# Optimization experiments

Hardware: AMD Instinct MI355X
Metric: run time of the kernel (lower is better)

The kernel has to match this reference:

```python
import jax, jax.numpy as jnp
import numpy as np
from jax import lax

D_MODEL, N_STATE, L_LEN = 1024, 64, 4096
DT_INIT = 0.1


def hippo_legs_matrix(N):
    # Standard HiPPO-LegS: A[n,k] = -sqrt(2n+1)sqrt(2k+1) if n>k, -(n+1) if n==k, 0 else
    n = np.arange(N, dtype=np.float32)
    r = np.sqrt(2.0 * n + 1.0)
    A = np.where(n[:, None] > n[None, :], r[:, None] * r[None, :], 0.0)
    A = -(A + np.diag(n + 1.0))
    B = r.copy()
    return jnp.asarray(A, jnp.float32), jnp.asarray(B, jnp.float32)


def setup_inputs() -> dict:
    key = jax.random.key(0)
    kB, kC = jax.random.split(key)
    A_ct, B_ref = hippo_legs_matrix(N_STATE)
    B0 = jnp.tile(B_ref[None, :], (D_MODEL, 1))
    B = B0 + 0.01 * jax.random.normal(kB, (D_MODEL, N_STATE), jnp.float32)
    C = jax.random.normal(kC, (D_MODEL, N_STATE), jnp.float32) * 0.1
    D = jnp.zeros((D_MODEL,), jnp.float32)
    log_dt = jnp.asarray(np.log(DT_INIT), jnp.float32)
    return {"A_ct": A_ct, "B": B, "C": C, "D": D, "log_dt": log_dt}


def reference(A_ct, B, C, D, log_dt):
    dt = jnp.exp(log_dt)
    N = A_ct.shape[0]
    I = jnp.eye(N, dtype=A_ct.dtype)
    M = I - (dt / 2.0) * A_ct          # (N,N)
    P = I + (dt / 2.0) * A_ct          # (N,N)
    A_bar = jnp.linalg.solve(M, P)     # (N,N)
    # B_bar[d] = M^{-1} (dt * B[d])  -> solve on transposed batch
    B_bar = jnp.linalg.solve(M, (dt * B).T).T  # (D,N)

    def step(x, _):
        # x: (D,N) state; emit readout then advance
        y = jnp.sum(C * x, axis=-1)    # (D,)
        return x @ A_bar.T, y

    _, ys = lax.scan(step, B_bar, None, length=L_LEN)  # ys: (L,D)
    K = ys.T                                           # (D,L)
    K = K.at[:, 0].add(D)
    return K[:, None, :]                                # (D,1,L)
```

## Files before the change

kernel.cpp:

```cpp
#include <hip/hip_runtime.h>
#include <math.h>


#define BPAD 72
#define ARR (64 * BPAD)

#define WS_BBAR   16
#define WS_SPL    65552
#define WS_MV     (WS_SPL + 12*8192)
#define WS_GT     (WS_MV + 4096)
#define WS_H      (WS_GT + 64*4096)
#define WS_W      (WS_H + 64*4096)
#define WS_X      (WS_W + 1024*4096)

using bf16x8 = __attribute__((ext_vector_type(8))) short;
using f32x4v = __attribute__((ext_vector_type(4))) float;
typedef unsigned short ushort_t;

__device__ __forceinline__ ushort_t f2bf(float x) {
  unsigned u = __builtin_bit_cast(unsigned, x);
  return (ushort_t)((u + 0x7FFFu + ((u >> 16) & 1u)) >> 16);
}
__device__ __forceinline__ float bfhi(float x) {
  unsigned u = __builtin_bit_cast(unsigned, x);
  unsigned r = (u + 0x7FFFu + ((u >> 16) & 1u)) & 0xFFFF0000u;
  return __builtin_bit_cast(float, r);
}
__device__ __forceinline__ ushort_t* usp(float* ws, int foff) {
  return (ushort_t*)(ws + foff);
}
__device__ __forceinline__ const ushort_t* uspc(const float* ws, int foff) {
  return (const ushort_t*)(ws + foff);
}

__device__ __forceinline__ void mm_frag(const ushort_t* __restrict__ Ah,
                                        const ushort_t* __restrict__ Al,
                                        const ushort_t* __restrict__ Bh,
                                        const ushort_t* __restrict__ Bl,
                                        int w, int lane, f32x4v acc[4]) {
  const int lm = lane & 15, quad = lane >> 4;
  const int ar = (16 * w + lm) * BPAD, ko = quad * 8;
#pragma unroll
  for (int nt = 0; nt < 4; ++nt) { acc[nt][0] = acc[nt][1] = acc[nt][2] = acc[nt][3] = 0.f; }
#pragma unroll
  for (int kc = 0; kc < 64; kc += 32) {
    const bf16x8 ahi = *(const bf16x8*)&Ah[ar + kc + ko];
    const bf16x8 alo = *(const bf16x8*)&Al[ar + kc + ko];
#pragma unroll
    for (int nt = 0; nt < 4; ++nt) {
      const int br = (16 * nt + lm) * BPAD + kc + ko;
      const bf16x8 bhi = *(const bf16x8*)&Bh[br];
      const bf16x8 blo = *(const bf16x8*)&Bl[br];
      acc[nt] = __builtin_amdgcn_mfma_f32_16x16x32_bf16(ahi, bhi, acc[nt], 0, 0, 0);
      acc[nt] = __builtin_amdgcn_mfma_f32_16x16x32_bf16(ahi, blo, acc[nt], 0, 0, 0);
      acc[nt] = __builtin_amdgcn_mfma_f32_16x16x32_bf16(alo, bhi, acc[nt], 0, 0, 0);
    }
  }
}

__device__ __forceinline__ void dstore_lds(const f32x4v acc[4],
                                           ushort_t* __restrict__ Ah, ushort_t* __restrict__ Al,
                                           ushort_t* __restrict__ Bth, ushort_t* __restrict__ Btl,
                                           int w, int lane) {
  const int lm = lane & 15, quad = lane >> 4;
  const int m0 = 16 * w + 4 * quad;
#pragma unroll
  for (int nt = 0; nt < 4; ++nt) {
    const int n = 16 * nt + lm;
    ushort_t h[4], l[4];
#pragma unroll
    for (int reg = 0; reg < 4; ++reg) {
      const float x = acc[nt][reg];
      h[reg] = f2bf(x); l[reg] = f2bf(x - bfhi(x));
      Ah[(m0 + reg) * BPAD + n] = h[reg];
      Al[(m0 + reg) * BPAD + n] = l[reg];
    }
    uint2 hp, lp;
    hp.x = (unsigned)h[0] | ((unsigned)h[1] << 16);
    hp.y = (unsigned)h[2] | ((unsigned)h[3] << 16);
    lp.x = (unsigned)l[0] | ((unsigned)l[1] << 16);
    lp.y = (unsigned)l[2] | ((unsigned)l[3] << 16);
    *(uint2*)&Bth[n * BPAD + m0] = hp;
    *(uint2*)&Btl[n * BPAD + m0] = lp;
  }
}

__device__ __forceinline__ void cp_l2w(const ushort_t* __restrict__ l,
                                       ushort_t* __restrict__ g, int tid) {
  for (int e = tid; e < 512; e += 256) {
    const int row = e >> 3, c8 = (e & 7) * 8;
    *(uint4*)&g[row * 64 + c8] = *(const uint4*)&l[row * BPAD + c8];
  }
}
__device__ __forceinline__ void cp_w2l(const ushort_t* __restrict__ g,
                                       ushort_t* __restrict__ l, int tid) {
  for (int e = tid; e < 512; e += 256) {
    const int row = e >> 3, c8 = (e & 7) * 8;
    *(uint4*)&l[row * BPAD + c8] = *(const uint4*)&g[row * 64 + c8];
  }
}

__device__ __forceinline__ void split_stage(const float* __restrict__ g,
                                            ushort_t* __restrict__ Ah,
                                            ushort_t* __restrict__ Al, int tid) {
#pragma unroll
  for (int j = 0; j < 4; ++j) {
    const int flat = j * 1024 + tid * 4;
    const int row = flat >> 6, col = flat & 63;
    const float4 v = *(const float4*)&g[flat];
    ushort_t h0 = f2bf(v.x), h1 = f2bf(v.y), h2 = f2bf(v.z), h3 = f2bf(v.w);
    ushort_t l0 = f2bf(v.x - bfhi(v.x)), l1 = f2bf(v.y - bfhi(v.y));
    ushort_t l2 = f2bf(v.z - bfhi(v.z)), l3 = f2bf(v.w - bfhi(v.w));
    uint2 hp, lp;
    hp.x = (unsigned)h0 | ((unsigned)h1 << 16); hp.y = (unsigned)h2 | ((unsigned)h3 << 16);
    lp.x = (unsigned)l0 | ((unsigned)l1 << 16); lp.y = (unsigned)l2 | ((unsigned)l3 << 16);
    *(uint2*)&Ah[row * BPAD + col] = hp;
    *(uint2*)&Al[row * BPAD + col] = lp;
  }
}

__global__ __launch_bounds__(256) void k_setup(const float* __restrict__ A,
                                               const float* __restrict__ logdt,
                                               float* __restrict__ ws) {
  __shared__ __align__(16) char SM[74240];
  float* Msh = (float*)SM;
  float* Tm  = (float*)(SM + 16640);
  float* tmpb = (float*)(SM + 33280);
  ushort_t* ping = (ushort_t*)(SM + 37376);
  ushort_t* pong = (ushort_t*)SM;
  const int tid = threadIdx.x;
  const int w = tid >> 6, lane = tid & 63;

  const float hdt = 0.5f * expf(logdt[0]);
  for (int idx = tid; idx < 4096; idx += 256) {
    const int i = idx >> 6, j = idx & 63;
    Msh[i * 65 + j] = ((i == j) ? 1.f : 0.f) - hdt * A[idx];
    Tm[i * 65 + j] = 0.f;
  }
  __syncthreads();
  if (tid < 64) Tm[tid * 65 + tid] = 1.0f / Msh[tid * 65 + tid];
  __syncthreads();
  for (int lb = 0; lb < 6; ++lb) {
    const int b = 1 << lb;
    const int E = 32 * b;
    for (int e = tid; e < E; e += 256) {
      const int rem = e & (b * b - 1);
      const int p = e >> (2 * lb);
      const int i = rem >> lb, j = rem & (b - 1);
      const int c0 = p << (lb + 1), r0 = c0 + b;
      float s = 0.f;
      for (int k = 0; k < b; ++k)
        s += Msh[(r0 + i) * 65 + c0 + k] * Tm[(c0 + k) * 65 + c0 + j];
      tmpb[e] = s;
    }
    __syncthreads();
    for (int e = tid; e < E; e += 256) {
      const int rem = e & (b * b - 1);
      const int p = e >> (2 * lb);
      const int i = rem >> lb, j = rem & (b - 1);
      const int c0 = p << (lb + 1), r0 = c0 + b;
      float s = 0.f;
      const float* tp = &tmpb[e - rem];
      for (int k = 0; k < b; ++k)
        s += Tm[(r0 + i) * 65 + r0 + k] * tp[k * b + j];
      Tm[(r0 + i) * 65 + c0 + j] = -s;
    }
    __syncthreads();
  }

  {
    ushort_t* MvH = usp(ws, WS_MV);
    ushort_t* MvL = usp(ws, WS_MV + 2048);
    for (int idx = tid; idx < 4096; idx += 256) {
      const int i = idx >> 6, j = idx & 63;
      const float mv = Tm[i * 65 + j];
      MvH[idx] = f2bf(mv); MvL[idx] = f2bf(mv - bfhi(mv));
      const float v = 2.f * mv - ((i == j) ? 1.f : 0.f);
      const ushort_t h = f2bf(v), l = f2bf(v - bfhi(v));
      ping[0 * ARR + i * BPAD + j] = h; ping[1 * ARR + i * BPAD + j] = l;
      ping[2 * ARR + j * BPAD + i] = h; ping[3 * ARR + j * BPAD + i] = l;
    }
  }
  __syncthreads();
  cp_l2w(ping + 0 * ARR, usp(ws, WS_SPL + 0), tid);
  cp_l2w(ping + 1 * ARR, usp(ws, WS_SPL + 2048), tid);
  cp_l2w(ping + 2 * ARR, usp(ws, WS_SPL + 4096), tid);
  cp_l2w(ping + 3 * ARR, usp(ws, WS_SPL + 6144), tid);

  ushort_t* cur = ping;
  ushort_t* nxt = pong;
  for (int sj = 1; sj < 12; ++sj) {
    f32x4v acc[4];
    mm_frag(cur, cur + ARR, cur + 2 * ARR, cur + 3 * ARR, w, lane, acc);
    dstore_lds(acc, nxt, nxt + ARR, nxt + 2 * ARR, nxt + 3 * ARR, w, lane);
    __syncthreads();
    const int base = WS_SPL + sj * 8192;
    cp_l2w(nxt + 0 * ARR, usp(ws, base + 0), tid);
    cp_l2w(nxt + 1 * ARR, usp(ws, base + 2048), tid);
    cp_l2w(nxt + 2 * ARR, usp(ws, base + 4096), tid);
    cp_l2w(nxt + 3 * ARR, usp(ws, base + 6144), tid);
    ushort_t* t = cur; cur = nxt; nxt = t;
  }
}

__global__ __launch_bounds__(256) void k_powers(const float* __restrict__ Bg,
                                                const float* __restrict__ logdt,
                                                float* __restrict__ ws) {
  __shared__ __align__(16) ushort_t SMp[8 * ARR];
  ushort_t* curA = SMp;
  ushort_t* ponA = SMp + 2 * ARR;
  ushort_t* Bst  = SMp + 4 * ARR;
  ushort_t* BtO  = SMp + 6 * ARR;
  const int p = blockIdx.x, tid = threadIdx.x;
  const int w = tid >> 6, lane = tid & 63;

  if (p < 128) {
    const int chain = p >> 6, r = p & 63;
    ushort_t* dstH = usp(ws, (chain ? WS_H : WS_GT) + r * 4096);
    ushort_t* dstL = usp(ws, (chain ? WS_H : WS_GT) + r * 4096 + 2048);
    if (r == 0) {
      for (int idx = tid; idx < 4096; idx += 256) {
        const int i = idx >> 6, j = idx & 63;
        dstH[idx] = (i == j) ? (ushort_t)0x3F80 : (ushort_t)0;
        dstL[idx] = 0;
      }
      return;
    }
    const int j0 = __ffs(r) - 1;
    if (r == (1 << j0)) {
      const int sb = WS_SPL + (chain * 6 + j0) * 8192;
      const int src = chain ? sb : (sb + 4096);
      const uint4* sh = (const uint4*)uspc(ws, src);
      const uint4* sl = (const uint4*)uspc(ws, src + 2048);
      uint4* dh = (uint4*)dstH;
      uint4* dl = (uint4*)dstL;
      for (int e = tid; e < 512; e += 256) { dh[e] = sh[e]; dl[e] = sl[e]; }
      return;
    }
    {
      const int sb = WS_SPL + (chain * 6 + j0) * 8192;
      cp_w2l(uspc(ws, sb + 0), curA, tid);
      cp_w2l(uspc(ws, sb + 2048), curA + ARR, tid);
    }
    ushort_t* ca = curA;
    ushort_t* na = ponA;
    for (int j = j0 + 1; j < 6; ++j) {
      if ((r >> j) & 1) {
        __syncthreads();
        const int sb = WS_SPL + (chain * 6 + j) * 8192;
        cp_w2l(uspc(ws, sb + 4096), Bst, tid);
        cp_w2l(uspc(ws, sb + 6144), Bst + ARR, tid);
        __syncthreads();
        f32x4v acc[4];
        mm_frag(ca, ca + ARR, Bst, Bst + ARR, w, lane, acc);
        dstore_lds(acc, na, na + ARR, BtO, BtO + ARR, w, lane);
        ushort_t* t = ca; ca = na; na = t;
      }
    }
    __syncthreads();
    if (chain == 0) {
      cp_l2w(BtO, dstH, tid);
      cp_l2w(BtO + ARR, dstL, tid);
    } else {
      cp_l2w(ca, dstH, tid);
      cp_l2w(ca + ARR, dstL, tid);
    }
  } else {
    const int d0 = (p - 128) * 64;
    const float dtv = expf(logdt[0]);
    split_stage(Bg + d0 * 64, curA, curA + ARR, tid);
    cp_w2l(uspc(ws, WS_MV), Bst, tid);
    cp_w2l(uspc(ws, WS_MV + 2048), Bst + ARR, tid);
    __syncthreads();
    f32x4v acc[4];
    mm_frag(curA, curA + ARR, Bst, Bst + ARR, w, lane, acc);
    const int lm = lane & 15, quad = lane >> 4;
    float* od = ws + WS_BBAR + d0 * 64;
#pragma unroll
    for (int nt = 0; nt < 4; ++nt)
#pragma unroll
      for (int reg = 0; reg < 4; ++reg)
        od[(16 * w + 4 * quad + reg) * 64 + 16 * nt + lm] = dtv * acc[nt][reg];
  }
}

__global__ __launch_bounds__(256) void k_expand(const float* __restrict__ Cg,
                                                float* __restrict__ ws) {
  __shared__ __align__(16) ushort_t SMe[4 * ARR];
  ushort_t* Asp = SMe;
  ushort_t* Bsp = SMe + 2 * ARR;
  const int p = blockIdx.x, tid = threadIdx.x;
  const int chain = p >> 10, rr = (p >> 4) & 63, dch = p & 15;
  const int w = tid >> 6, lane = tid & 63;
  const int d0 = dch * 64;

  split_stage(chain ? (ws + WS_BBAR + d0 * 64) : (Cg + d0 * 64), Asp, Asp + ARR, tid);
  const int mb = (chain ? WS_H : WS_GT) + rr * 4096;
  cp_w2l(uspc(ws, mb + 0), Bsp, tid);
  cp_w2l(uspc(ws, mb + 2048), Bsp + ARR, tid);
  __syncthreads();

  f32x4v acc[4];
  mm_frag(Asp, Asp + ARR, Bsp, Bsp + ARR, w, lane, acc);

  const int lm = lane & 15, quad = lane >> 4;
  float* dst = ws + (chain ? WS_X : WS_W) + d0 * 4096 + rr * 64;
#pragma unroll
  for (int nt = 0; nt < 4; ++nt)
#pragma unroll
    for (int reg = 0; reg < 4; ++reg)
      dst[(16 * w + 4 * quad + reg) * 4096 + 16 * nt + lm] = acc[nt][reg];
}

__global__ __launch_bounds__(256) void k_contract(const float* __restrict__ Dg,
                                                  const float* __restrict__ ws,
                                                  float* __restrict__ out) {
  __shared__ __align__(16) ushort_t XhiL[64 * BPAD];
  __shared__ __align__(16) ushort_t XloL[64 * BPAD];
  __shared__ __align__(16) ushort_t WhiL[64 * BPAD];
  __shared__ __align__(16) ushort_t WloL[64 * BPAD];
  const int d = blockIdx.x, tid = threadIdx.x;
  const float* Wg = ws + WS_W + d * 4096;
  const float* Xg = ws + WS_X + d * 4096;

#pragma unroll
  for (int j = 0; j < 4; ++j) {
    const int flat = j * 1024 + tid * 4;
    const int row = flat >> 6, col = flat & 63;
    const float4 wv = *(const float4*)&Wg[flat];
    const float4 xv = *(const float4*)&Xg[flat];
    const int o = row * BPAD + col;
#pragma unroll
    for (int s = 0; s < 2; ++s) {
      const float4 v = s ? xv : wv;
      ushort_t h0 = f2bf(v.x), h1 = f2bf(v.y), h2 = f2bf(v.z), h3 = f2bf(v.w);
      ushort_t l0 = f2bf(v.x - bfhi(v.x)), l1 = f2bf(v.y - bfhi(v.y));
      ushort_t l2 = f2bf(v.z - bfhi(v.z)), l3 = f2bf(v.w - bfhi(v.w));
      uint2 hp, lp;
      hp.x = (unsigned)h0 | ((unsigned)h1 << 16); hp.y = (unsigned)h2 | ((unsigned)h3 << 16);
      lp.x = (unsigned)l0 | ((unsigned)l1 << 16); lp.y = (unsigned)l2 | ((unsigned)l3 << 16);
      *(uint2*)&(s ? XhiL : WhiL)[o] = hp;
      *(uint2*)&(s ? XloL : WloL)[o] = lp;
    }
  }
  __syncthreads();

  const int w = tid >> 6, lane = tid & 63;
  const int lm = lane & 15, quad = lane >> 4;
  const int qrow = 16 * w + lm;
  const int koff = quad * 8;

  f32x4v acc[4];
#pragma unroll
  for (int nt = 0; nt < 4; ++nt) { acc[nt][0] = 0.f; acc[nt][1] = 0.f; acc[nt][2] = 0.f; acc[nt][3] = 0.f; }

#pragma unroll
  for (int kc = 0; kc < 64; kc += 32) {
    const bf16x8 ahi = *(const bf16x8*)&XhiL[qrow * BPAD + kc + koff];
    const bf16x8 alo = *(const bf16x8*)&XloL[qrow * BPAD + kc + koff];
#pragma unroll
    for (int nt = 0; nt < 4; ++nt) {
      const int rrow = 16 * nt + lm;
      const bf16x8 bhi = *(const bf16x8*)&WhiL[rrow * BPAD + kc + koff];
      const bf16x8 blo = *(const bf16x8*)&WloL[rrow * BPAD + kc + koff];
      acc[nt] = __builtin_amdgcn_mfma_f32_16x16x32_bf16(ahi, bhi, acc[nt], 0, 0, 0);
      acc[nt] = __builtin_amdgcn_mfma_f32_16x16x32_bf16(ahi, blo, acc[nt], 0, 0, 0);
      acc[nt] = __builtin_amdgcn_mfma_f32_16x16x32_bf16(alo, bhi, acc[nt], 0, 0, 0);
    }
  }

  if (tid == 0) acc[0][0] += Dg[d];

  float* od = out + d * 4096;
#pragma unroll
  for (int nt = 0; nt < 4; ++nt) {
#pragma unroll
    for (int reg = 0; reg < 4; ++reg) {
      const int q = 16 * w + quad * 4 + reg;
      od[q * 64 + 16 * nt + lm] = acc[nt][reg];
    }
  }
}

extern "C" void kernel_launch(void* const* d_in, const int* in_sizes, int n_in,
                              void* d_out, int out_size, void* d_ws, size_t ws_size,
                              hipStream_t stream) {
  const float* A     = (const float*)d_in[0];
  const float* B     = (const float*)d_in[1];
  const float* C     = (const float*)d_in[2];
  const float* Dv    = (const float*)d_in[3];
  const float* logdt = (const float*)d_in[4];
  float* ws  = (float*)d_ws;
  float* out = (float*)d_out;

  hipLaunchKernelGGL(k_setup,    dim3(1),    dim3(256), 0, stream, A, logdt, ws);
  hipLaunchKernelGGL(k_powers,   dim3(144),  dim3(256), 0, stream, B, logdt, ws);
  hipLaunchKernelGGL(k_expand,   dim3(2048), dim3(256), 0, stream, C, ws);
  hipLaunchKernelGGL(k_contract, dim3(1024), dim3(256), 0, stream, Dv, ws, out);
}
```

Baseline: 127.2 us.

## Fuse four stage kernels into one cooperative persistent kernel with grid syncs

```diff
diff --git a/kernel.cpp b/kernel.cpp
--- a/kernel.cpp
+++ b/kernel.cpp
@@ -1,5 +1,8 @@
 #include <hip/hip_runtime.h>
+#include <hip/hip_cooperative_groups.h>
 #include <math.h>
+
+namespace cg = cooperative_groups;
 
 
 #define BPAD 72
@@ -74,6 +77,47 @@
       h[reg] = f2bf(x); l[reg] = f2bf(x - bfhi(x));
       Ah[(m0 + reg) * BPAD + n] = h[reg];
       Al[(m0 + reg) * BPAD + n] = l[reg];
+    }
+    uint2 hp, lp;
+    hp.x = (unsigned)h[0] | ((unsigned)h[1] << 16);
+    hp.y = (unsigned)h[2] | ((unsigned)h[3] << 16);
+    lp.x = (unsigned)l[0] | ((unsigned)l[1] << 16);
+    lp.y = (unsigned)l[2] | ((unsigned)l[3] << 16);
+    *(uint2*)&Bth[n * BPAD + m0] = hp;
+    *(uint2*)&Btl[n * BPAD + m0] = lp;
+  }
+}
+
+__device__ __forceinline__ void dstore_A(const f32x4v acc[4],
+                                         ushort_t* __restrict__ Ah, ushort_t* __restrict__ Al,
+                                         int w, int lane) {
+  const int lm = lane & 15, quad = lane >> 4;
+  const int m0 = 16 * w + 4 * quad;
+#pragma unroll
+  for (int nt = 0; nt < 4; ++nt) {
+    const int n = 16 * nt + lm;
+#pragma unroll
+    for (int reg = 0; reg < 4; ++reg) {
+      const float x = acc[nt][reg];
+      Ah[(m0 + reg) * BPAD + n] = f2bf(x);
+      Al[(m0 + reg) * BPAD + n] = f2bf(x - bfhi(x));
+    }
+  }
+}
+
+__device__ __forceinline__ void dstore_Bt(const f32x4v acc[4],
+                                          ushort_t* __restrict__ Bth, ushort_t* __restrict__ Btl,
+                                          int w, int lane) {
+  const int lm = lane & 15, quad = lane >> 4;
+  const int m0 = 16 * w + 4 * quad;
+#pragma unroll
+  for (int nt = 0; nt < 4; ++nt) {
+    const int n = 16 * nt + lm;
+    ushort_t h[4], l[4];
+#pragma unroll
+    for (int reg = 0; reg < 4; ++reg) {
+      const float x = acc[nt][reg];
+      h[reg] = f2bf(x); l[reg] = f2bf(x - bfhi(x));
     }
     uint2 hp, lp;
     hp.x = (unsigned)h[0] | ((unsigned)h[1] << 16);
@@ -119,103 +163,110 @@
   }
 }
 
-__global__ __launch_bounds__(256) void k_setup(const float* __restrict__ A,
-                                               const float* __restrict__ logdt,
-                                               float* __restrict__ ws) {
-  __shared__ __align__(16) char SM[74240];
-  float* Msh = (float*)SM;
-  float* Tm  = (float*)(SM + 16640);
-  float* tmpb = (float*)(SM + 33280);
-  ushort_t* ping = (ushort_t*)(SM + 37376);
-  ushort_t* pong = (ushort_t*)SM;
-  const int tid = threadIdx.x;
+__global__ __launch_bounds__(256, 4) void k_fused(const float* __restrict__ A,
+                                                  const float* __restrict__ Bg,
+                                                  const float* __restrict__ Cg,
+                                                  const float* __restrict__ Dg,
+                                                  const float* __restrict__ logdt,
+                                                  float* __restrict__ ws,
+                                                  float* __restrict__ out,
+                                                  int grid) {
+  __shared__ __align__(16) char SM[37376];
+  const int bid = blockIdx.x, tid = threadIdx.x;
   const int w = tid >> 6, lane = tid & 63;
-
-  const float hdt = 0.5f * expf(logdt[0]);
-  for (int idx = tid; idx < 4096; idx += 256) {
-    const int i = idx >> 6, j = idx & 63;
-    Msh[i * 65 + j] = ((i == j) ? 1.f : 0.f) - hdt * A[idx];
-    Tm[i * 65 + j] = 0.f;
-  }
-  __syncthreads();
-  if (tid < 64) Tm[tid * 65 + tid] = 1.0f / Msh[tid * 65 + tid];
-  __syncthreads();
-  for (int lb = 0; lb < 6; ++lb) {
-    const int b = 1 << lb;
-    const int E = 32 * b;
-    for (int e = tid; e < E; e += 256) {
-      const int rem = e & (b * b - 1);
-      const int p = e >> (2 * lb);
-      const int i = rem >> lb, j = rem & (b - 1);
-      const int c0 = p << (lb + 1), r0 = c0 + b;
-      float s = 0.f;
-      for (int k = 0; k < b; ++k)
-        s += Msh[(r0 + i) * 65 + c0 + k] * Tm[(c0 + k) * 65 + c0 + j];
-      tmpb[e] = s;
-    }
-    __syncthreads();
-    for (int e = tid; e < E; e += 256) {
-      const int rem = e & (b * b - 1);
-      const int p = e >> (2 * lb);
-      const int i = rem >> lb, j = rem & (b - 1);
-      const int c0 = p << (lb + 1), r0 = c0 + b;
-      float s = 0.f;
-      const float* tp = &tmpb[e - rem];
-      for (int k = 0; k < b; ++k)
-        s += Tm[(r0 + i) * 65 + r0 + k] * tp[k * b + j];
-      Tm[(r0 + i) * 65 + c0 + j] = -s;
-    }
-    __syncthreads();
-  }
-
-  {
+  cg::grid_group gg = cg::this_grid();
+
+  if (bid == 0) {
+    float* Msh = (float*)SM;
+    float* Tm  = (float*)(SM + 16640);
+    float* tmpb = (float*)(SM + 33280);
+    ushort_t* ping = (ushort_t*)SM;
+
+    const float hdt = 0.5f * expf(logdt[0]);
+    for (int idx = tid; idx < 4096; idx += 256) {
+      const int i = idx >> 6, j = idx & 63;
+      Msh[i * 65 + j] = ((i == j) ? 1.f : 0.f) - hdt * A[idx];
+      Tm[i * 65 + j] = 0.f;
+    }
+    __syncthreads();
+    if (tid < 64) Tm[tid * 65 + tid] = 1.0f / Msh[tid * 65 + tid];
+    __syncthreads();
+    for (int lb = 0; lb < 6; ++lb) {
+      const int b = 1 << lb;
+      const int E = 32 * b;
+      for (int e = tid; e < E; e += 256) {
+        const int rem = e & (b * b - 1);
+        const int p = e >> (2 * lb);
+        const int i = rem >> lb, j = rem & (b - 1);
+        const int c0 = p << (lb + 1), r0 = c0 + b;
+        float s = 0.f;
+        for (int k = 0; k < b; ++k)
+          s += Msh[(r0 + i) * 65 + c0 + k] * Tm[(c0 + k) * 65 + c0 + j];
+        tmpb[e] = s;
+      }
+      __syncthreads();
+      for (int e = tid; e < E; e += 256) {
+        const int rem = e & (b * b - 1);
+        const int p = e >> (2 * lb);
+        const int i = rem >> lb, j = rem & (b - 1);
+        const int c0 = p << (lb + 1), r0 = c0 + b;
+        float s = 0.f;
+        const float* tp = &tmpb[e - rem];
+        for (int k = 0; k < b; ++k)
+          s += Tm[(r0 + i) * 65 + r0 + k] * tp[k * b + j];
+        Tm[(r0 + i) * 65 + c0 + j] = -s;
+      }
+      __syncthreads();
+    }
+
     ushort_t* MvH = usp(ws, WS_MV);
     ushort_t* MvL = usp(ws, WS_MV + 2048);
-    for (int idx = tid; idx < 4096; idx += 256) {
+    float mv[16];
+#pragma unroll
+    for (int t16 = 0; t16 < 16; ++t16) {
+      const int idx = tid + 256 * t16;
+      const float m = Tm[(idx >> 6) * 65 + (idx & 63)];
+      mv[t16] = m;
+      MvH[idx] = f2bf(m); MvL[idx] = f2bf(m - bfhi(m));
+    }
+    __syncthreads();
+#pragma unroll
+    for (int t16 = 0; t16 < 16; ++t16) {
+      const int idx = tid + 256 * t16;
       const int i = idx >> 6, j = idx & 63;
-      const float mv = Tm[i * 65 + j];
-      MvH[idx] = f2bf(mv); MvL[idx] = f2bf(mv - bfhi(mv));
-      const float v = 2.f * mv - ((i == j) ? 1.f : 0.f);
-      const ushort_t h = f2bf(v), l = f2bf(v - bfhi(v));
-      ping[0 * ARR + i * BPAD + j] = h; ping[1 * ARR + i * BPAD + j] = l;
-      ping[2 * ARR + j * BPAD + i] = h; ping[3 * ARR + j * BPAD + i] = l;
-    }
-  }
-  __syncthreads();
-  cp_l2w(ping + 0 * ARR, usp(ws, WS_SPL + 0), tid);
-  cp_l2w(ping + 1 * ARR, usp(ws, WS_SPL + 2048), tid);
-  cp_l2w(ping + 2 * ARR, usp(ws, WS_SPL + 4096), tid);
-  cp_l2w(ping + 3 * ARR, usp(ws, WS_SPL + 6144), tid);
-
-  ushort_t* cur = ping;
-  ushort_t* nxt = pong;
-  for (int sj = 1; sj < 12; ++sj) {
-    f32x4v acc[4];
-    mm_frag(cur, cur + ARR, cur + 2 * ARR, cur + 3 * ARR, w, lane, acc);
-    dstore_lds(acc, nxt, nxt + ARR, nxt + 2 * ARR, nxt + 3 * ARR, w, lane);
-    __syncthreads();
-    const int base = WS_SPL + sj * 8192;
-    cp_l2w(nxt + 0 * ARR, usp(ws, base + 0), tid);
-    cp_l2w(nxt + 1 * ARR, usp(ws, base + 2048), tid);
-    cp_l2w(nxt + 2 * ARR, usp(ws, base + 4096), tid);
-    cp_l2w(nxt + 3 * ARR, usp(ws, base + 6144), tid);
-    ushort_t* t = cur; cur = nxt; nxt = t;
-  }
-}
-
-__global__ __launch_bounds__(256) void k_powers(const float* __restrict__ Bg,
-                                                const float* __restrict__ logdt,
-                                                float* __restrict__ ws) {
-  __shared__ __align__(16) ushort_t SMp[8 * ARR];
-  ushort_t* curA = SMp;
-  ushort_t* ponA = SMp + 2 * ARR;
-  ushort_t* Bst  = SMp + 4 * ARR;
-  ushort_t* BtO  = SMp + 6 * ARR;
-  const int p = blockIdx.x, tid = threadIdx.x;
-  const int w = tid >> 6, lane = tid & 63;
-
-  if (p < 128) {
-    const int chain = p >> 6, r = p & 63;
+      const float v = 2.f * mv[t16] - ((i == j) ? 1.f : 0.f);
+      const ushort_t h = f2bf(v), l2 = f2bf(v - bfhi(v));
+      ping[0 * ARR + i * BPAD + j] = h; ping[1 * ARR + i * BPAD + j] = l2;
+      ping[2 * ARR + j * BPAD + i] = h; ping[3 * ARR + j * BPAD + i] = l2;
+    }
+    __syncthreads();
+    cp_l2w(ping + 0 * ARR, usp(ws, WS_SPL + 0), tid);
+    cp_l2w(ping + 1 * ARR, usp(ws, WS_SPL + 2048), tid);
+    cp_l2w(ping + 2 * ARR, usp(ws, WS_SPL + 4096), tid);
+    cp_l2w(ping + 3 * ARR, usp(ws, WS_SPL + 6144), tid);
+
+    for (int sj = 1; sj < 12; ++sj) {
+      f32x4v acc[4];
+      mm_frag(ping, ping + ARR, ping + 2 * ARR, ping + 3 * ARR, w, lane, acc);
+      __syncthreads();
+      dstore_lds(acc, ping, ping + ARR, ping + 2 * ARR, ping + 3 * ARR, w, lane);
+      __syncthreads();
+      const int base = WS_SPL + sj * 8192;
+      cp_l2w(ping + 0 * ARR, usp(ws, base + 0), tid);
+      cp_l2w(ping + 1 * ARR, usp(ws, base + 2048), tid);
+      cp_l2w(ping + 2 * ARR, usp(ws, base + 4096), tid);
+      cp_l2w(ping + 3 * ARR, usp(ws, base + 6144), tid);
+    }
+  }
+  __threadfence();
+  gg.sync();
+  __threadfence();
+
+  ushort_t* ca  = (ushort_t*)SM;
+  ushort_t* Bst = (ushort_t*)SM + 2 * ARR;
+
+  if (bid < 128) {
+    const int chain = bid >> 6, r = bid & 63;
     ushort_t* dstH = usp(ws, (chain ? WS_H : WS_GT) + r * 4096);
     ushort_t* dstL = usp(ws, (chain ? WS_H : WS_GT) + r * 4096 + 2048);
     if (r == 0) {
@@ -224,56 +275,51 @@
         dstH[idx] = (i == j) ? (ushort_t)0x3F80 : (ushort_t)0;
         dstL[idx] = 0;
       }
-      return;
-    }
-    const int j0 = __ffs(r) - 1;
-    if (r == (1 << j0)) {
-      const int sb = WS_SPL + (chain * 6 + j0) * 8192;
-      const int src = chain ? sb : (sb + 4096);
-      const uint4* sh = (const uint4*)uspc(ws, src);
-      const uint4* sl = (const uint4*)uspc(ws, src + 2048);
-      uint4* dh = (uint4*)dstH;
-      uint4* dl = (uint4*)dstL;
-      for (int e = tid; e < 512; e += 256) { dh[e] = sh[e]; dl[e] = sl[e]; }
-      return;
-    }
-    {
-      const int sb = WS_SPL + (chain * 6 + j0) * 8192;
-      cp_w2l(uspc(ws, sb + 0), curA, tid);
-      cp_w2l(uspc(ws, sb + 2048), curA + ARR, tid);
-    }
-    ushort_t* ca = curA;
-    ushort_t* na = ponA;
-    for (int j = j0 + 1; j < 6; ++j) {
-      if ((r >> j) & 1) {
+    } else {
+      const int j0 = __ffs(r) - 1;
+      if (r == (1 << j0)) {
+        const int sb = WS_SPL + (chain * 6 + j0) * 8192;
+        const int src = chain ? sb : (sb + 4096);
+        const uint4* sh = (const uint4*)uspc(ws, src);
+        const uint4* sl = (const uint4*)uspc(ws, src + 2048);
+        uint4* dh = (uint4*)dstH;
+        uint4* dl = (uint4*)dstL;
+        for (int e = tid; e < 512; e += 256) { dh[e] = sh[e]; dl[e] = sl[e]; }
+      } else {
+        const int sb0 = WS_SPL + (chain * 6 + j0) * 8192;
+        cp_w2l(uspc(ws, sb0 + 0), ca, tid);
+        cp_w2l(uspc(ws, sb0 + 2048), ca + ARR, tid);
+        for (int j = j0 + 1; j < 6; ++j) {
+          if ((r >> j) & 1) {
+            __syncthreads();
+            const int sb = WS_SPL + (chain * 6 + j) * 8192;
+            cp_w2l(uspc(ws, sb + 4096), Bst, tid);
+            cp_w2l(uspc(ws, sb + 6144), Bst + ARR, tid);
+            __syncthreads();
+            f32x4v acc[4];
+            mm_frag(ca, ca + ARR, Bst, Bst + ARR, w, lane, acc);
+            __syncthreads();
+            const bool last = ((r >> (j + 1)) == 0);
+            if (last && chain == 0)
+              dstore_Bt(acc, Bst, Bst + ARR, w, lane);
+            else
+              dstore_A(acc, ca, ca + ARR, w, lane);
+          }
+        }
         __syncthreads();
-        const int sb = WS_SPL + (chain * 6 + j) * 8192;
-        cp_w2l(uspc(ws, sb + 4096), Bst, tid);
-        cp_w2l(uspc(ws, sb + 6144), Bst + ARR, tid);
-        __syncthreads();
-        f32x4v acc[4];
-        mm_frag(ca, ca + ARR, Bst, Bst + ARR, w, lane, acc);
-        dstore_lds(acc, na, na + ARR, BtO, BtO + ARR, w, lane);
-        ushort_t* t = ca; ca = na; na = t;
-      }
-    }
-    __syncthreads();
-    if (chain == 0) {
-      cp_l2w(BtO, dstH, tid);
-      cp_l2w(BtO + ARR, dstL, tid);
-    } else {
-      cp_l2w(ca, dstH, tid);
-      cp_l2w(ca + ARR, dstL, tid);
-    }
-  } else {
-    const int d0 = (p - 128) * 64;
+        if (chain == 0) { cp_l2w(Bst, dstH, tid); cp_l2w(Bst + ARR, dstL, tid); }
+        else           { cp_l2w(ca, dstH, tid);  cp_l2w(ca + ARR, dstL, tid); }
+      }
+    }
+  } else if (bid < 144) {
+    const int d0 = (bid - 128) * 64;
     const float dtv = expf(logdt[0]);
-    split_stage(Bg + d0 * 64, curA, curA + ARR, tid);
+    split_stage(Bg + d0 * 64, ca, ca + ARR, tid);
     cp_w2l(uspc(ws, WS_MV), Bst, tid);
     cp_w2l(uspc(ws, WS_MV + 2048), Bst + ARR, tid);
     __syncthreads();
     f32x4v acc[4];
-    mm_frag(curA, curA + ARR, Bst, Bst + ARR, w, lane, acc);
+    mm_frag(ca, ca + ARR, Bst, Bst + ARR, w, lane, acc);
     const int lm = lane & 15, quad = lane >> 4;
     float* od = ws + WS_BBAR + d0 * 64;
 #pragma unroll
@@ -282,103 +328,94 @@
       for (int reg = 0; reg < 4; ++reg)
         od[(16 * w + 4 * quad + reg) * 64 + 16 * nt + lm] = dtv * acc[nt][reg];
   }
-}
-
-__global__ __launch_bounds__(256) void k_expand(const float* __restrict__ Cg,
-                                                float* __restrict__ ws) {
-  __shared__ __align__(16) ushort_t SMe[4 * ARR];
-  ushort_t* Asp = SMe;
-  ushort_t* Bsp = SMe + 2 * ARR;
-  const int p = blockIdx.x, tid = threadIdx.x;
-  const int chain = p >> 10, rr = (p >> 4) & 63, dch = p & 15;
-  const int w = tid >> 6, lane = tid & 63;
-  const int d0 = dch * 64;
-
-  split_stage(chain ? (ws + WS_BBAR + d0 * 64) : (Cg + d0 * 64), Asp, Asp + ARR, tid);
-  const int mb = (chain ? WS_H : WS_GT) + rr * 4096;
-  cp_w2l(uspc(ws, mb + 0), Bsp, tid);
-  cp_w2l(uspc(ws, mb + 2048), Bsp + ARR, tid);
-  __syncthreads();
-
-  f32x4v acc[4];
-  mm_frag(Asp, Asp + ARR, Bsp, Bsp + ARR, w, lane, acc);
-
-  const int lm = lane & 15, quad = lane >> 4;
-  float* dst = ws + (chain ? WS_X : WS_W) + d0 * 4096 + rr * 64;
-#pragma unroll
-  for (int nt = 0; nt < 4; ++nt)
-#pragma unroll
-    for (int reg = 0; reg < 4; ++reg)
-      dst[(16 * w + 4 * quad + reg) * 4096 + 16 * nt + lm] = acc[nt][reg];
-}
-
-__global__ __launch_bounds__(256) void k_contract(const float* __restrict__ Dg,
-                                                  const float* __restrict__ ws,
-                                                  float* __restrict__ out) {
-  __shared__ __align__(16) ushort_t XhiL[64 * BPAD];
-  __shared__ __align__(16) ushort_t XloL[64 * BPAD];
-  __shared__ __align__(16) ushort_t WhiL[64 * BPAD];
-  __shared__ __align__(16) ushort_t WloL[64 * BPAD];
-  const int d = blockIdx.x, tid = threadIdx.x;
-  const float* Wg = ws + WS_W + d * 4096;
-  const float* Xg = ws + WS_X + d * 4096;
-
-#pragma unroll
-  for (int j = 0; j < 4; ++j) {
-    const int flat = j * 1024 + tid * 4;
-    const int row = flat >> 6, col = flat & 63;
-    const float4 wv = *(const float4*)&Wg[flat];
-    const float4 xv = *(const float4*)&Xg[flat];
-    const int o = row * BPAD + col;
-#pragma unroll
-    for (int s = 0; s < 2; ++s) {
-      const float4 v = s ? xv : wv;
-      ushort_t h0 = f2bf(v.x), h1 = f2bf(v.y), h2 = f2bf(v.z), h3 = f2bf(v.w);
-      ushort_t l0 = f2bf(v.x - bfhi(v.x)), l1 = f2bf(v.y - bfhi(v.y));
-      ushort_t l2 = f2bf(v.z - bfhi(v.z)), l3 = f2bf(v.w - bfhi(v.w));
-      uint2 hp, lp;
-      hp.x = (unsigned)h0 | ((unsigned)h1 << 16); hp.y = (unsigned)h2 | ((unsigned)h3 << 16);
-      lp.x = (unsigned)l0 | ((unsigned)l1 << 16); lp.y = (unsigned)l2 | ((unsigned)l3 << 16);
-      *(uint2*)&(s ? XhiL : WhiL)[o] = hp;
-      *(uint2*)&(s ? XloL : WloL)[o] = lp;
-    }
-  }
-  __syncthreads();
-
-  const int w = tid >> 6, lane = tid & 63;
-  const int lm = lane & 15, quad = lane >> 4;
-  const int qrow = 16 * w + lm;
-  const int koff = quad * 8;
-
-  f32x4v acc[4];
-#pragma unroll
-  for (int nt = 0; nt < 4; ++nt) { acc[nt][0] = 0.f; acc[nt][1] = 0.f; acc[nt][2] = 0.f; acc[nt][3] = 0.f; }
-
-#pragma unroll
-  for (int kc = 0; kc < 64; kc += 32) {
-    const bf16x8 ahi = *(const bf16x8*)&XhiL[qrow * BPAD + kc + koff];
-    const bf16x8 alo = *(const bf16x8*)&XloL[qrow * BPAD + kc + koff];
+  __threadfence();
+  gg.sync();
+  __threadfence();
+
+  for (int t = bid; t < 2048; t += grid) {
+    const int chain = t >> 10, rr = (t >> 4) & 63, dch = t & 15;
+    const int d0 = dch * 64;
+    split_stage(chain ? (ws + WS_BBAR + d0 * 64) : (Cg + d0 * 64), ca, ca + ARR, tid);
+    const int mb = (chain ? WS_H : WS_GT) + rr * 4096;
+    cp_w2l(uspc(ws, mb + 0), Bst, tid);
+    cp_w2l(uspc(ws, mb + 2048), Bst + ARR, tid);
+    __syncthreads();
+    f32x4v acc[4];
+    mm_frag(ca, ca + ARR, Bst, Bst + ARR, w, lane, acc);
+    const int lm = lane & 15, quad = lane >> 4;
+    float* dst = ws + (chain ? WS_X : WS_W) + d0 * 4096 + rr * 64;
+#pragma unroll
+    for (int nt = 0; nt < 4; ++nt)
+#pragma unroll
+      for (int reg = 0; reg < 4; ++reg)
+        dst[(16 * w + 4 * quad + reg) * 4096 + 16 * nt + lm] = acc[nt][reg];
+    __syncthreads();
+  }
+  __threadfence();
+  gg.sync();
+  __threadfence();
+
+  ushort_t* XhiL = (ushort_t*)SM;
+  ushort_t* XloL = XhiL + ARR;
+  ushort_t* WhiL = XhiL + 2 * ARR;
+  ushort_t* WloL = XhiL + 3 * ARR;
+  for (int t = bid; t < 1024; t += grid) {
+    const float* Wg = ws + WS_W + t * 4096;
+    const float* Xg = ws + WS_X + t * 4096;
+#pragma unroll
+    for (int j = 0; j < 4; ++j) {
+      const int flat = j * 1024 + tid * 4;
+      const int row = flat >> 6, col = flat & 63;
+      const float4 wv = *(const float4*)&Wg[flat];
+      const float4 xv = *(const float4*)&Xg[flat];
+      const int o = row * BPAD + col;
+#pragma unroll
+      for (int s = 0; s < 2; ++s) {
+        const float4 v = s ? xv : wv;
+        ushort_t h0 = f2bf(v.x), h1 = f2bf(v.y), h2 = f2bf(v.z), h3 = f2bf(v.w);
+        ushort_t l0 = f2bf(v.x - bfhi(v.x)), l1 = f2bf(v.y - bfhi(v.y));
+        ushort_t l2 = f2bf(v.z - bfhi(v.z)), l3 = f2bf(v.w - bfhi(v.w));
+        uint2 hp, lp;
+        hp.x = (unsigned)h0 | ((unsigned)h1 << 16); hp.y = (unsigned)h2 | ((unsigned)h3 << 16);
+        lp.x = (unsigned)l0 | ((unsigned)l1 << 16); lp.y = (unsigned)l2 | ((unsigned)l3 << 16);
+        *(uint2*)&(s ? XhiL : WhiL)[o] = hp;
+        *(uint2*)&(s ? XloL : WloL)[o] = lp;
+      }
+    }
+    __syncthreads();
+
+    const int lm = lane & 15, quad = lane >> 4;
+    const int qrow = 16 * w + lm;
+    const int koff = quad * 8;
+    f32x4v acc[4];
+#pragma unroll
+    for (int nt = 0; nt < 4; ++nt) { acc[nt][0] = 0.f; acc[nt][1] = 0.f; acc[nt][2] = 0.f; acc[nt][3] = 0.f; }
+#pragma unroll
+    for (int kc = 0; kc < 64; kc += 32) {
+      const bf16x8 ahi = *(const bf16x8*)&XhiL[qrow * BPAD + kc + koff];
+      const bf16x8 alo = *(const bf16x8*)&XloL[qrow * BPAD + kc + koff];
+#pragma unroll
+      for (int nt = 0; nt < 4; ++nt) {
+        const int rrow = 16 * nt + lm;
+        const bf16x8 bhi = *(const bf16x8*)&WhiL[rrow * BPAD + kc + koff];
+        const bf16x8 blo = *(const bf16x8*)&WloL[rrow * BPAD + kc + koff];
+        acc[nt] = __builtin_amdgcn_mfma_f32_16x16x32_bf16(ahi, bhi, acc[nt], 0, 0, 0);
+        acc[nt] = __builtin_amdgcn_mfma_f32_16x16x32_bf16(ahi, blo, acc[nt], 0, 0, 0);
+        acc[nt] = __builtin_amdgcn_mfma_f32_16x16x32_bf16(alo, bhi, acc[nt], 0, 0, 0);
+      }
+    }
+    if (tid == 0) acc[0][0] += Dg[t];
+
+    float* od = out + t * 4096;
 #pragma unroll
     for (int nt = 0; nt < 4; ++nt) {
-      const int rrow = 16 * nt + lm;
-      const bf16x8 bhi = *(const bf16x8*)&WhiL[rrow * BPAD + kc + koff];
-      const bf16x8 blo = *(const bf16x8*)&WloL[rrow * BPAD + kc + koff];
-      acc[nt] = __builtin_amdgcn_mfma_f32_16x16x32_bf16(ahi, bhi, acc[nt], 0, 0, 0);
-      acc[nt] = __builtin_amdgcn_mfma_f32_16x16x32_bf16(ahi, blo, acc[nt], 0, 0, 0);
-      acc[nt] = __builtin_amdgcn_mfma_f32_16x16x32_bf16(alo, bhi, acc[nt], 0, 0, 0);
-    }
-  }
-
-  if (tid == 0) acc[0][0] += Dg[d];
-
-  float* od = out + d * 4096;
-#pragma unroll
-  for (int nt = 0; nt < 4; ++nt) {
-#pragma unroll
-    for (int reg = 0; reg < 4; ++reg) {
-      const int q = 16 * w + quad * 4 + reg;
-      od[q * 64 + 16 * nt + lm] = acc[nt][reg];
-    }
+#pragma unroll
+      for (int reg = 0; reg < 4; ++reg) {
+        const int q = 16 * w + quad * 4 + reg;
+        od[q * 64 + 16 * nt + lm] = acc[nt][reg];
+      }
+    }
+    __syncthreads();
   }
 }
 
@@ -393,8 +430,17 @@
   float* ws  = (float*)d_ws;
   float* out = (float*)d_out;
 
-  hipLaunchKernelGGL(k_setup,    dim3(1),    dim3(256), 0, stream, A, logdt, ws);
-  hipLaunchKernelGGL(k_powers,   dim3(144),  dim3(256), 0, stream, B, logdt, ws);
-  hipLaunchKernelGGL(k_expand,   dim3(2048), dim3(256), 0, stream, C, ws);
-  hipLaunchKernelGGL(k_contract, dim3(1024), dim3(256), 0, stream, Dv, ws, out);
-}
+  static int grid_blocks = 0;
+  if (grid_blocks == 0) {
+    int nb = 0;
+    if (hipOccupancyMaxActiveBlocksPerMultiprocessor(&nb, k_fused, 256, 0) != hipSuccess || nb < 1)
+      nb = 2;
+    int g = nb * 256;
+    if (g > 1024) g = 1024;
+    grid_blocks = g;
+  }
+  int grid = grid_blocks;
+  void* args[] = {(void*)&A, (void*)&B, (void*)&C, (void*)&Dv,
+                  (void*)&logdt, (void*)&ws, (void*)&out, (void*)&grid};
+  hipLaunchCooperativeKernel(k_fused, dim3(grid), dim3(256), args, 0, stream);
+}
```

Measured after the change: 505.4 us. 297% more time.

## Use 1024-thread blocks with one 16x16 tile per wave in setup and powers

Applied to the files above, without the earlier changes.

```diff
diff --git a/kernel.cpp b/kernel.cpp
--- a/kernel.cpp
+++ b/kernel.cpp
@@ -58,43 +58,95 @@
   }
 }
 
-__device__ __forceinline__ void dstore_lds(const f32x4v acc[4],
+__device__ __forceinline__ void mm_frag16(const ushort_t* __restrict__ Ah,
+                                          const ushort_t* __restrict__ Al,
+                                          const ushort_t* __restrict__ Bh,
+                                          const ushort_t* __restrict__ Bl,
+                                          int mt, int nt, int lane, f32x4v& acc) {
+  const int lm = lane & 15, quad = lane >> 4;
+  const int ar = (16 * mt + lm) * BPAD, br = (16 * nt + lm) * BPAD, ko = quad * 8;
+  acc[0] = acc[1] = acc[2] = acc[3] = 0.f;
+#pragma unroll
+  for (int kc = 0; kc < 64; kc += 32) {
+    const bf16x8 ahi = *(const bf16x8*)&Ah[ar + kc + ko];
+    const bf16x8 alo = *(const bf16x8*)&Al[ar + kc + ko];
+    const bf16x8 bhi = *(const bf16x8*)&Bh[br + kc + ko];
+    const bf16x8 blo = *(const bf16x8*)&Bl[br + kc + ko];
+    acc = __builtin_amdgcn_mfma_f32_16x16x32_bf16(ahi, bhi, acc, 0, 0, 0);
+    acc = __builtin_amdgcn_mfma_f32_16x16x32_bf16(ahi, blo, acc, 0, 0, 0);
+    acc = __builtin_amdgcn_mfma_f32_16x16x32_bf16(alo, bhi, acc, 0, 0, 0);
+  }
+}
+
+__device__ __forceinline__ void dstore_lds16(const f32x4v& acc,
+                                             ushort_t* __restrict__ Ah, ushort_t* __restrict__ Al,
+                                             ushort_t* __restrict__ Bth, ushort_t* __restrict__ Btl,
+                                             int mt, int nt, int lane) {
+  const int lm = lane & 15, quad = lane >> 4;
+  const int m0 = 16 * mt + 4 * quad;
+  const int n = 16 * nt + lm;
+  ushort_t h[4], l[4];
+#pragma unroll
+  for (int reg = 0; reg < 4; ++reg) {
+    const float x = acc[reg];
+    h[reg] = f2bf(x); l[reg] = f2bf(x - bfhi(x));
+    Ah[(m0 + reg) * BPAD + n] = h[reg];
+    Al[(m0 + reg) * BPAD + n] = l[reg];
+  }
+  uint2 hp, lp;
+  hp.x = (unsigned)h[0] | ((unsigned)h[1] << 16);
+  hp.y = (unsigned)h[2] | ((unsigned)h[3] << 16);
+  lp.x = (unsigned)l[0] | ((unsigned)l[1] << 16);
+  lp.y = (unsigned)l[2] | ((unsigned)l[3] << 16);
+  *(uint2*)&Bth[n * BPAD + m0] = hp;
+  *(uint2*)&Btl[n * BPAD + m0] = lp;
+}
+
+__device__ __forceinline__ void dstore_A16(const f32x4v& acc,
                                            ushort_t* __restrict__ Ah, ushort_t* __restrict__ Al,
-                                           ushort_t* __restrict__ Bth, ushort_t* __restrict__ Btl,
-                                           int w, int lane) {
-  const int lm = lane & 15, quad = lane >> 4;
-  const int m0 = 16 * w + 4 * quad;
-#pragma unroll
-  for (int nt = 0; nt < 4; ++nt) {
-    const int n = 16 * nt + lm;
-    ushort_t h[4], l[4];
-#pragma unroll
-    for (int reg = 0; reg < 4; ++reg) {
-      const float x = acc[nt][reg];
-      h[reg] = f2bf(x); l[reg] = f2bf(x - bfhi(x));
-      Ah[(m0 + reg) * BPAD + n] = h[reg];
-      Al[(m0 + reg) * BPAD + n] = l[reg];
-    }
-    uint2 hp, lp;
-    hp.x = (unsigned)h[0] | ((unsigned)h[1] << 16);
-    hp.y = (unsigned)h[2] | ((unsigned)h[3] << 16);
-    lp.x = (unsigned)l[0] | ((unsigned)l[1] << 16);
-    lp.y = (unsigned)l[2] | ((unsigned)l[3] << 16);
-    *(uint2*)&Bth[n * BPAD + m0] = hp;
-    *(uint2*)&Btl[n * BPAD + m0] = lp;
-  }
+                                           int mt, int nt, int lane) {
+  const int lm = lane & 15, quad = lane >> 4;
+  const int m0 = 16 * mt + 4 * quad;
+  const int n = 16 * nt + lm;
+#pragma unroll
+  for (int reg = 0; reg < 4; ++reg) {
+    const float x = acc[reg];
+    Ah[(m0 + reg) * BPAD + n] = f2bf(x);
+    Al[(m0 + reg) * BPAD + n] = f2bf(x - bfhi(x));
+  }
+}
+
+__device__ __forceinline__ void dstore_Bt16(const f32x4v& acc,
+                                            ushort_t* __restrict__ Bth, ushort_t* __restrict__ Btl,
+                                            int mt, int nt, int lane) {
+  const int lm = lane & 15, quad = lane >> 4;
+  const int m0 = 16 * mt + 4 * quad;
+  const int n = 16 * nt + lm;
+  ushort_t h[4], l[4];
+#pragma unroll
+  for (int reg = 0; reg < 4; ++reg) {
+    const float x = acc[reg];
+    h[reg] = f2bf(x); l[reg] = f2bf(x - bfhi(x));
+  }
+  uint2 hp, lp;
+  hp.x = (unsigned)h[0] | ((unsigned)h[1] << 16);
+  hp.y = (unsigned)h[2] | ((unsigned)h[3] << 16);
+  lp.x = (unsigned)l[0] | ((unsigned)l[1] << 16);
+  lp.y = (unsigned)l[2] | ((unsigned)l[3] << 16);
+  *(uint2*)&Bth[n * BPAD + m0] = hp;
+  *(uint2*)&Btl[n * BPAD + m0] = lp;
 }
 
 __device__ __forceinline__ void cp_l2w(const ushort_t* __restrict__ l,
-                                       ushort_t* __restrict__ g, int tid) {
-  for (int e = tid; e < 512; e += 256) {
+                                       ushort_t* __restrict__ g, int tid, int NT) {
+  for (int e = tid; e < 512; e += NT) {
     const int row = e >> 3, c8 = (e & 7) * 8;
     *(uint4*)&g[row * 64 + c8] = *(const uint4*)&l[row * BPAD + c8];
   }
 }
 __device__ __forceinline__ void cp_w2l(const ushort_t* __restrict__ g,
-                                       ushort_t* __restrict__ l, int tid) {
-  for (int e = tid; e < 512; e += 256) {
+                                       ushort_t* __restrict__ l, int tid, int NT) {
+  for (int e = tid; e < 512; e += NT) {
     const int row = e >> 3, c8 = (e & 7) * 8;
     *(uint4*)&l[row * BPAD + c8] = *(const uint4*)&g[row * 64 + c8];
   }
@@ -102,10 +154,8 @@
 
 __device__ __forceinline__ void split_stage(const float* __restrict__ g,
                                             ushort_t* __restrict__ Ah,
-                                            ushort_t* __restrict__ Al, int tid) {
-#pragma unroll
-  for (int j = 0; j < 4; ++j) {
-    const int flat = j * 1024 + tid * 4;
+                                            ushort_t* __restrict__ Al, int tid, int NT) {
+  for (int flat = tid * 4; flat < 4096; flat += NT * 4) {
     const int row = flat >> 6, col = flat & 63;
     const float4 v = *(const float4*)&g[flat];
     ushort_t h0 = f2bf(v.x), h1 = f2bf(v.y), h2 = f2bf(v.z), h3 = f2bf(v.w);
@@ -119,20 +169,22 @@
   }
 }
 
-__global__ __launch_bounds__(256) void k_setup(const float* __restrict__ A,
-                                               const float* __restrict__ logdt,
-                                               float* __restrict__ ws) {
-  __shared__ __align__(16) char SM[74240];
+__global__ __launch_bounds__(1024) void k_setup(const float* __restrict__ A,
+                                                const float* __restrict__ logdt,
+                                                float* __restrict__ ws) {
+  __shared__ __align__(16) char SM[73728];
   float* Msh = (float*)SM;
   float* Tm  = (float*)(SM + 16640);
   float* tmpb = (float*)(SM + 33280);
-  ushort_t* ping = (ushort_t*)(SM + 37376);
-  ushort_t* pong = (ushort_t*)SM;
+  ushort_t* ping = (ushort_t*)SM;
+  ushort_t* pong = (ushort_t*)(SM + 36864);
   const int tid = threadIdx.x;
   const int w = tid >> 6, lane = tid & 63;
+  const int mt = w >> 2, nt = w & 3;
+  const int NT = 1024;
 
   const float hdt = 0.5f * expf(logdt[0]);
-  for (int idx = tid; idx < 4096; idx += 256) {
+  for (int idx = tid; idx < 4096; idx += NT) {
     const int i = idx >> 6, j = idx & 63;
     Msh[i * 65 + j] = ((i == j) ? 1.f : 0.f) - hdt * A[idx];
     Tm[i * 65 + j] = 0.f;
@@ -143,7 +195,7 @@
   for (int lb = 0; lb < 6; ++lb) {
     const int b = 1 << lb;
     const int E = 32 * b;
-    for (int e = tid; e < E; e += 256) {
+    for (int e = tid; e < E; e += NT) {
       const int rem = e & (b * b - 1);
       const int p = e >> (2 * lb);
       const int i = rem >> lb, j = rem & (b - 1);
@@ -154,7 +206,7 @@
       tmpb[e] = s;
     }
     __syncthreads();
-    for (int e = tid; e < E; e += 256) {
+    for (int e = tid; e < E; e += NT) {
       const int rem = e & (b * b - 1);
       const int p = e >> (2 * lb);
       const int i = rem >> lb, j = rem & (b - 1);
@@ -171,55 +223,64 @@
   {
     ushort_t* MvH = usp(ws, WS_MV);
     ushort_t* MvL = usp(ws, WS_MV + 2048);
-    for (int idx = tid; idx < 4096; idx += 256) {
+    float mv[4];
+#pragma unroll
+    for (int t4 = 0; t4 < 4; ++t4) {
+      const int idx = tid + NT * t4;
+      const float m = Tm[(idx >> 6) * 65 + (idx & 63)];
+      mv[t4] = m;
+      MvH[idx] = f2bf(m); MvL[idx] = f2bf(m - bfhi(m));
+    }
+    __syncthreads();
+#pragma unroll
+    for (int t4 = 0; t4 < 4; ++t4) {
+      const int idx = tid + NT * t4;
       const int i = idx >> 6, j = idx & 63;
-      const float mv = Tm[i * 65 + j];
-      MvH[idx] = f2bf(mv); MvL[idx] = f2bf(mv - bfhi(mv));
-      const float v = 2.f * mv - ((i == j) ? 1.f : 0.f);
-      const ushort_t h = f2bf(v), l = f2bf(v - bfhi(v));
-      ping[0 * ARR + i * BPAD + j] = h; ping[1 * ARR + i * BPAD + j] = l;
-      ping[2 * ARR + j * BPAD + i] = h; ping[3 * ARR + j * BPAD + i] = l;
+      const float v = 2.f * mv[t4] - ((i == j) ? 1.f : 0.f);
+      const ushort_t h = f2bf(v), l2 = f2bf(v - bfhi(v));
+      ping[0 * ARR + i * BPAD + j] = h; ping[1 * ARR + i * BPAD + j] = l2;
+      ping[2 * ARR + j * BPAD + i] = h; ping[3 * ARR + j * BPAD + i] = l2;
     }
   }
   __syncthreads();
-  cp_l2w(ping + 0 * ARR, usp(ws, WS_SPL + 0), tid);
-  cp_l2w(ping + 1 * ARR, usp(ws, WS_SPL + 2048), tid);
-  cp_l2w(ping + 2 * ARR, usp(ws, WS_SPL + 4096), tid);
-  cp_l2w(ping + 3 * ARR, usp(ws, WS_SPL + 6144), tid);
+  cp_l2w(ping + 0 * ARR, usp(ws, WS_SPL + 0), tid, NT);
+  cp_l2w(ping + 1 * ARR, usp(ws, WS_SPL + 2048), tid, NT);
+  cp_l2w(ping + 2 * ARR, usp(ws, WS_SPL + 4096), tid, NT);
+  cp_l2w(ping + 3 * ARR, usp(ws, WS_SPL + 6144), tid, NT);
 
   ushort_t* cur = ping;
   ushort_t* nxt = pong;
   for (int sj = 1; sj < 12; ++sj) {
-    f32x4v acc[4];
-    mm_frag(cur, cur + ARR, cur + 2 * ARR, cur + 3 * ARR, w, lane, acc);
-    dstore_lds(acc, nxt, nxt + ARR, nxt + 2 * ARR, nxt + 3 * ARR, w, lane);
+    f32x4v acc;
+    mm_frag16(cur, cur + ARR, cur + 2 * ARR, cur + 3 * ARR, mt, nt, lane, acc);
+    dstore_lds16(acc, nxt, nxt + ARR, nxt + 2 * ARR, nxt + 3 * ARR, mt, nt, lane);
     __syncthreads();
     const int base = WS_SPL + sj * 8192;
-    cp_l2w(nxt + 0 * ARR, usp(ws, base + 0), tid);
-    cp_l2w(nxt + 1 * ARR, usp(ws, base + 2048), tid);
-    cp_l2w(nxt + 2 * ARR, usp(ws, base + 4096), tid);
-    cp_l2w(nxt + 3 * ARR, usp(ws, base + 6144), tid);
+    cp_l2w(nxt + 0 * ARR, usp(ws, base + 0), tid, NT);
+    cp_l2w(nxt + 1 * ARR, usp(ws, base + 2048), tid, NT);
+    cp_l2w(nxt + 2 * ARR, usp(ws, base + 4096), tid, NT);
+    cp_l2w(nxt + 3 * ARR, usp(ws, base + 6144), tid, NT);
     ushort_t* t = cur; cur = nxt; nxt = t;
   }
 }
 
-__global__ __launch_bounds__(256) void k_powers(const float* __restrict__ Bg,
-                                                const float* __restrict__ logdt,
-                                                float* __restrict__ ws) {
-  __shared__ __align__(16) ushort_t SMp[8 * ARR];
-  ushort_t* curA = SMp;
-  ushort_t* ponA = SMp + 2 * ARR;
-  ushort_t* Bst  = SMp + 4 * ARR;
-  ushort_t* BtO  = SMp + 6 * ARR;
+__global__ __launch_bounds__(1024) void k_powers(const float* __restrict__ Bg,
+                                                 const float* __restrict__ logdt,
+                                                 float* __restrict__ ws) {
+  __shared__ __align__(16) ushort_t SMp[4 * ARR];
+  ushort_t* ca  = SMp;
+  ushort_t* Bst = SMp + 2 * ARR;
   const int p = blockIdx.x, tid = threadIdx.x;
   const int w = tid >> 6, lane = tid & 63;
+  const int mt = w >> 2, nt = w & 3;
+  const int NT = 1024;
 
   if (p < 128) {
     const int chain = p >> 6, r = p & 63;
     ushort_t* dstH = usp(ws, (chain ? WS_H : WS_GT) + r * 4096);
     ushort_t* dstL = usp(ws, (chain ? WS_H : WS_GT) + r * 4096 + 2048);
     if (r == 0) {
-      for (int idx = tid; idx < 4096; idx += 256) {
+      for (int idx = tid; idx < 4096; idx += NT) {
         const int i = idx >> 6, j = idx & 63;
         dstH[idx] = (i == j) ? (ushort_t)0x3F80 : (ushort_t)0;
         dstL[idx] = 0;
@@ -234,53 +295,48 @@
       const uint4* sl = (const uint4*)uspc(ws, src + 2048);
       uint4* dh = (uint4*)dstH;
       uint4* dl = (uint4*)dstL;
-      for (int e = tid; e < 512; e += 256) { dh[e] = sh[e]; dl[e] = sl[e]; }
+      for (int e = tid; e < 512; e += NT) { dh[e] = sh[e]; dl[e] = sl[e]; }
       return;
     }
     {
-      const int sb = WS_SPL + (chain * 6 + j0) * 8192;
-      cp_w2l(uspc(ws, sb + 0), curA, tid);
-      cp_w2l(uspc(ws, sb + 2048), curA + ARR, tid);
-    }
-    ushort_t* ca = curA;
-    ushort_t* na = ponA;
+      const int sb0 = WS_SPL + (chain * 6 + j0) * 8192;
+      cp_w2l(uspc(ws, sb0 + 0), ca, tid, NT);
+      cp_w2l(uspc(ws, sb0 + 2048), ca + ARR, tid, NT);
+    }
     for (int j = j0 + 1; j < 6; ++j) {
       if ((r >> j) & 1) {
         __syncthreads();
         const int sb = WS_SPL + (chain * 6 + j) * 8192;
-        cp_w2l(uspc(ws, sb + 4096), Bst, tid);
-        cp_w2l(uspc(ws, sb + 6144), Bst + ARR, tid);
+        cp_w2l(uspc(ws, sb + 4096), Bst, tid, NT);
+        cp_w2l(uspc(ws, sb + 6144), Bst + ARR, tid, NT);
         __syncthreads();
-        f32x4v acc[4];
-        mm_frag(ca, ca + ARR, Bst, Bst + ARR, w, lane, acc);
-        dstore_lds(acc, na, na + ARR, BtO, BtO + ARR, w, lane);
-        ushort_t* t = ca; ca = na; na = t;
+        f32x4v acc;
+        mm_frag16(ca, ca + ARR, Bst, Bst + ARR, mt, nt, lane, acc);
+        __syncthreads();
+        const bool last = ((r >> (j + 1)) == 0);
+        if (last && chain == 0)
+          dstore_Bt16(acc, Bst, Bst + ARR, mt, nt, lane);
+        else
+          dstore_A16(acc, ca, ca + ARR, mt, nt, lane);
       }
     }
     __syncthreads();
-    if (chain == 0) {
-      cp_l2w(BtO, dstH, tid);
-      cp_l2w(BtO + ARR, dstL, tid);
-    } else {
-      cp_l2w(ca, dstH, tid);
-      cp_l2w(ca + ARR, dstL, tid);
-    }
+    if (chain == 0) { cp_l2w(Bst, dstH, tid, NT); cp_l2w(Bst + ARR, dstL, tid, NT); }
+    else            { cp_l2w(ca, dstH, tid, NT);  cp_l2w(ca + ARR, dstL, tid, NT); }
   } else {
     const int d0 = (p - 128) * 64;
     const float dtv = expf(logdt[0]);
-    split_stage(Bg + d0 * 64, curA, curA + ARR, tid);
-    cp_w2l(uspc(ws, WS_MV), Bst, tid);
-    cp_w2l(uspc(ws, WS_MV + 2048), Bst + ARR, tid);
-    __syncthreads();
-    f32x4v acc[4];
-    mm_frag(curA, curA + ARR, Bst, Bst + ARR, w, lane, acc);
+    split_stage(Bg + d0 * 64, ca, ca + ARR, tid, NT);
+    cp_w2l(uspc(ws, WS_MV), Bst, tid, NT);
+    cp_w2l(uspc(ws, WS_MV + 2048), Bst + ARR, tid, NT);
+    __syncthreads();
+    f32x4v acc;
+    mm_frag16(ca, ca + ARR, Bst, Bst + ARR, mt, nt, lane, acc);
     const int lm = lane & 15, quad = lane >> 4;
     float* od = ws + WS_BBAR + d0 * 64;
 #pragma unroll
-    for (int nt = 0; nt < 4; ++nt)
-#pragma unroll
-      for (int reg = 0; reg < 4; ++reg)
-        od[(16 * w + 4 * quad + reg) * 64 + 16 * nt + lm] = dtv * acc[nt][reg];
+    for (int reg = 0; reg < 4; ++reg)
+      od[(16 * mt + 4 * quad + reg) * 64 + 16 * nt + lm] = dtv * acc[reg];
   }
 }
 
@@ -294,10 +350,10 @@
   const int w = tid >> 6, lane = tid & 63;
   const int d0 = dch * 64;
 
-  split_stage(chain ? (ws + WS_BBAR + d0 * 64) : (Cg + d0 * 64), Asp, Asp + ARR, tid);
+  split_stage(chain ? (ws + WS_BBAR + d0 * 64) : (Cg + d0 * 64), Asp, Asp + ARR, tid, 256);
   const int mb = (chain ? WS_H : WS_GT) + rr * 4096;
-  cp_w2l(uspc(ws, mb + 0), Bsp, tid);
-  cp_w2l(uspc(ws, mb + 2048), Bsp + ARR, tid);
+  cp_w2l(uspc(ws, mb + 0), Bsp, tid, 256);
+  cp_w2l(uspc(ws, mb + 2048), Bsp + ARR, tid, 256);
   __syncthreads();
 
   f32x4v acc[4];
@@ -393,8 +449,8 @@
   float* ws  = (float*)d_ws;
   float* out = (float*)d_out;
 
-  hipLaunchKernelGGL(k_setup,    dim3(1),    dim3(256), 0, stream, A, logdt, ws);
-  hipLaunchKernelGGL(k_powers,   dim3(144),  dim3(256), 0, stream, B, logdt, ws);
-  hipLaunchKernelGGL(k_expand,   dim3(2048), dim3(256), 0, stream, C, ws);
-  hipLaunchKernelGGL(k_contract, dim3(1024), dim3(256), 0, stream, Dv, ws, out);
-}
+  hipLaunchKernelGGL(k_setup,    dim3(1),    dim3(1024), 0, stream, A, logdt, ws);
+  hipLaunchKernelGGL(k_powers,   dim3(144),  dim3(1024), 0, stream, B, logdt, ws);
+  hipLaunchKernelGGL(k_expand,   dim3(2048), dim3(256),  0, stream, C, ws);
+  hipLaunchKernelGGL(k_contract, dim3(1024), dim3(256),  0, stream, Dv, ws, out);
+}
```

After: 119.6 us. 1.06x faster.
